# Performance work log

Hardware: AMD Instinct MI355X
Metric: run time of the kernel (lower is better)

Reference implementation:

```python
import jax, jax.numpy as jnp
import numpy as np

H_DIM = 256
N_HEADS = 8
HALF = H_DIM // 2

def _lin(x, W, b):
    # torch nn.Linear: y = x @ W.T + b
    y = x @ W.T
    return y + b if b is not None else y

def setup_inputs() -> dict:
    key = jax.random.key(0)
    ks = jax.random.split(key, 16)
    s = 0.02
    d = {
        'x': jax.random.normal(ks[0], (16, H_DIM, 32, 32), jnp.float32),
        'q1_w': jax.random.normal(ks[1], (HALF, HALF), jnp.float32) * s,
        'q1_b': jnp.zeros((HALF,), jnp.float32),
        'q2_w': jax.random.normal(ks[2], (HALF, HALF), jnp.float32) * s,
        'q2_b': jnp.zeros((HALF,), jnp.float32),
        'k1_w': jax.random.normal(ks[3], (HALF, HALF), jnp.float32) * s,
        'k1_b': jnp.zeros((HALF,), jnp.float32),
        'k2_w': jax.random.normal(ks[4], (HALF, HALF), jnp.float32) * s,
        'k2_b': jnp.zeros((HALF,), jnp.float32),
        'v1_w': jax.random.normal(ks[5], (HALF, HALF), jnp.float32) * s,
        'v1_b': jnp.zeros((HALF,), jnp.float32),
        'v2_w': jax.random.normal(ks[6], (HALF, HALF), jnp.float32) * s,
        'v2_b': jnp.zeros((HALF,), jnp.float32),
        'proj1_w': jax.random.normal(ks[7], (HALF, HALF), jnp.float32) * s,
        'proj1_b': jnp.zeros((HALF,), jnp.float32),
        'proj2_w': jax.random.normal(ks[8], (HALF, HALF), jnp.float32) * s,
        'proj2_b': jnp.zeros((HALF,), jnp.float32),
        'logit_scale': jnp.log(10.0 * jnp.ones((N_HEADS, 1, 1), jnp.float32)),
        'mlp_w1': jax.random.normal(ks[9], (128, 2), jnp.float32) * s,
        'mlp_b1': jnp.zeros((128,), jnp.float32),
        'mlp_w2': jax.random.normal(ks[10], (N_HEADS, 128), jnp.float32) * s,
    }
    return d

def _rel_pos_index(h, w):
    # static (numpy) relative position index, shape [N, N]
    ch, cw = np.meshgrid(np.arange(h), np.arange(w), indexing='ij')
    coords = np.stack([ch.reshape(-1), cw.reshape(-1)])  # [2, N]
    rel = coords[:, :, None] - coords[:, None, :]         # [2, N, N]
    rel = rel.transpose(1, 2, 0)
    rel[:, :, 0] += h - 1
    rel[:, :, 1] += w - 1
    return rel[:, :, 0] * (2 * w - 1) + rel[:, :, 1]

def _forward(x, q1_w, q1_b, q2_w, q2_b, k1_w, k1_b, k2_w, k2_b,
             v1_w, v1_b, v2_w, v2_b, proj1_w, proj1_b, proj2_w, proj2_b,
             logit_scale, mlp_w1, mlp_b1, mlp_w2):
    b, c, h, w = x.shape
    N = h * w
    nh = N_HEADS
    hd = c // nh
    x3 = jnp.transpose(x, (0, 2, 3, 1)).reshape(b, N, c)
    x0, x1 = x3[..., :c // 2], x3[..., c // 2:]

    def qkv(W0, b0, W1, b1):
        t = jnp.concatenate([x0 + _lin(x0, W0, b0), x1 + _lin(x1, W1, b1)], axis=-1)
        return t.reshape(b, N, nh, hd).transpose(0, 2, 1, 3)  # [b, nh, N, hd]

    q = qkv(q1_w, q1_b, q2_w, q2_b)
    k = qkv(k1_w, k1_b, k2_w, k2_b)
    v = qkv(v1_w, v1_b, v2_w, v2_b)

    eps = 1e-12
    qn = q / jnp.maximum(jnp.linalg.norm(q, axis=-1, keepdims=True), eps)
    kn = k / jnp.maximum(jnp.linalg.norm(k, axis=-1, keepdims=True), eps)
    attn = jnp.einsum('bhnd,bhmd->bhnm', qn, kn)  # cosine similarity
    scale = jnp.exp(jnp.minimum(logit_scale, jnp.log(1.0 / 0.01)))  # [nh,1,1]
    attn = attn * scale[None]

    # continuous relative-position bias (CPB) table via small MLP
    rch = jnp.arange(-(h - 1), h, dtype=jnp.float32) / (h - 1 + 1e-8)
    rcw = jnp.arange(-(w - 1), w, dtype=jnp.float32) / (w - 1 + 1e-8)
    gh, gw = jnp.meshgrid(rch, rcw, indexing='ij')
    tab = jnp.stack([gh, gw], axis=-1) * 3.2               # [2h-1, 2w-1, 2]
    tab = jnp.sign(tab) * (1.0 - jnp.exp(-jnp.abs(tab)))
    tab = jax.nn.relu(_lin(tab, mlp_w1, mlp_b1))
    tab = _lin(tab, mlp_w2, None).reshape(-1, nh)          # [(2h-1)(2w-1), nh]

    idx = jnp.asarray(_rel_pos_index(h, w))                # [N, N]
    bias = tab[idx.reshape(-1)].reshape(N, N, nh).transpose(2, 0, 1)
    bias = 16.0 * jax.nn.sigmoid(bias)
    attn = attn + bias[None]

    attn = jax.nn.softmax(attn, axis=-1)
    out = jnp.einsum('bhnm,bhmd->bhnd', attn, v).transpose(0, 2, 1, 3).reshape(b, N, c)
    o0, o1 = out[..., :c // 2], out[..., c // 2:]
    out = jnp.concatenate([_lin(o0, proj1_w, proj1_b), _lin(o1, proj2_w, proj2_b)], axis=-1)
    return out.reshape(b, h, w, c).transpose(0, 3, 1, 2)

def reference(x, q1_w, q1_b, q2_w, q2_b, k1_w, k1_b, k2_w, k2_b,
              v1_w, v1_b, v2_w, v2_b, proj1_w, proj1_b, proj2_w, proj2_b,
              logit_scale, mlp_w1, mlp_b1, mlp_w2):
    return _forward(x, q1_w, q1_b, q2_w, q2_b, k1_w, k1_b, k2_w, k2_b,
                    v1_w, v1_b, v2_w, v2_b, proj1_w, proj1_b, proj2_w, proj2_b,
                    logit_scale, mlp_w1, mlp_b1, mlp_w2)
```

## Files before the change

### kernel.cpp

```cpp
#include <hip/hip_runtime.h>
#include <cmath>


typedef _Float16 half_t;
typedef __attribute__((ext_vector_type(4))) _Float16 half4;
typedef __attribute__((ext_vector_type(8))) _Float16 half8;
typedef __attribute__((ext_vector_type(4))) float float4v;

static __device__ __forceinline__ float4v mfma16(half8 a, half8 b, float4v c) {
  return __builtin_amdgcn_mfma_f32_16x16x32_f16(a, b, c, 0, 0, 0);
}

struct PtrArr8 { const float* p[8]; };

__global__ __launch_bounds__(256) void prep_w(PtrArr8 wsrc, PtrArr8 bsrc,
                                              half_t* __restrict__ wf,
                                              float* __restrict__ bws) {
  int y = blockIdx.y;
  const float* src = nullptr;
  const float* bs = nullptr;
#pragma unroll
  for (int i = 0; i < 8; i++)
    if (i == y) { src = wsrc.p[i]; bs = bsrc.p[i]; }
  int i0 = (blockIdx.x * 256 + threadIdx.x) * 4;
  float4 w = *(const float4*)(src + i0);
  int j = i0 >> 7, k = i0 & 127;
  float id0 = 0.f, id1 = 0.f, id2 = 0.f, id3 = 0.f;
  if (y < 6) {
    if (j == k)     id0 = 1.0f;
    if (j == k + 1) id1 = 1.0f;
    if (j == k + 2) id2 = 1.0f;
    if (j == k + 3) id3 = 1.0f;
  }
  half4 h;
  h[0] = (half_t)(w.x + id0);
  h[1] = (half_t)(w.y + id1);
  h[2] = (half_t)(w.z + id2);
  h[3] = (half_t)(w.w + id3);
  *(half4*)(wf + y * 16384 + i0) = h;
  if (blockIdx.x == 0 && threadIdx.x < 128)
    bws[y * 128 + threadIdx.x] = bs[threadIdx.x];
}

__global__ __launch_bounds__(256) void bias_mlp(const float* __restrict__ w1,
                                                const float* __restrict__ b1,
                                                const float* __restrict__ w2,
                                                float* __restrict__ tabh) {
  __shared__ float sw1[256];
  __shared__ float sb1[128];
  __shared__ float sw2[1024];
  int t = threadIdx.x;
  sw1[t] = w1[t];
  if (t < 128) sb1[t] = b1[t];
  for (int i = t; i < 1024; i += 256) sw2[i] = w2[i];
  __syncthreads();
  int p = blockIdx.x * 256 + t;
  if (p >= 3969) return;
  int ph = p / 63, pw = p % 63;
  float t0 = (float)(ph - 31) * (3.2f / 31.0f);
  float t1 = (float)(pw - 31) * (3.2f / 31.0f);
  t0 = copysignf(1.0f - __expf(-fabsf(t0)), t0);
  t1 = copysignf(1.0f - __expf(-fabsf(t1)), t1);
  float acc[8];
#pragma unroll
  for (int hh = 0; hh < 8; hh++) acc[hh] = 0.0f;
  for (int j = 0; j < 128; j++) {
    float hj = fmaxf(0.0f, t0 * sw1[2 * j] + t1 * sw1[2 * j + 1] + sb1[j]);
#pragma unroll
    for (int hh = 0; hh < 8; hh++) acc[hh] += hj * sw2[hh * 128 + j];
  }
#pragma unroll
  for (int hh = 0; hh < 8; hh++)
    tabh[hh * 3969 + p] = 16.0f / (1.0f + __expf(-acc[hh]));
}

__global__ __launch_bounds__(256) void qkv_mfma(
    const float* __restrict__ x, const half_t* __restrict__ wf,
    const float* __restrict__ lscale, const float* __restrict__ bws,
    half_t* __restrict__ qf, half_t* __restrict__ kf,
    half_t* __restrict__ vf) {
  __shared__ half_t wb[128 * 136];
  __shared__ half_t tbuf[128 * 68];
  int t = threadIdx.x;
  int lane = t & 63, wv = t >> 6, l = lane & 15, quad = lane >> 4;
  int hf = blockIdx.y;
  int m0 = blockIdx.x * 64;
  int b = m0 >> 10, n0 = m0 & 1023;

  half8 afr[4];
  {
    const float* xb = x + (size_t)b * 256 * 1024 + n0 + wv * 16 + l;
#pragma unroll
    for (int ks = 0; ks < 4; ks++) {
      int kbase = hf * 128 + ks * 32 + quad * 8;
      half8 a;
#pragma unroll
      for (int j = 0; j < 8; j++)
        a[j] = (half_t)xb[(size_t)(kbase + j) * 1024];
      afr[ks] = a;
    }
  }

  for (int op = 0; op < 3; op++) {
    int combo = op * 2 + hf;
    __syncthreads();
    {
      const half_t* wg = wf + combo * 16384;
#pragma unroll
      for (int i = 0; i < 8; i++) {
        int flat = (t + 256 * i) * 8;
        int row = flat >> 7, col = flat & 127;
        *(half8*)(wb + row * 136 + col) = *(const half8*)(wg + flat);
      }
    }
    __syncthreads();

    float4v acc[8];
#pragma unroll
    for (int ng = 0; ng < 8; ng++) {
      float4v c = {0.f, 0.f, 0.f, 0.f};
#pragma unroll
      for (int ks = 0; ks < 4; ks++) {
        half8 bfrag =
            *(const half8*)(wb + (ng * 16 + l) * 136 + ks * 32 + quad * 8);
        c = mfma16(afr[ks], bfrag, c);
      }
      acc[ng] = c;
    }
#pragma unroll
    for (int ng = 0; ng < 8; ng++) {
      float bb = bws[combo * 128 + ng * 16 + l];
#pragma unroll
      for (int r2 = 0; r2 < 4; r2++) acc[ng][r2] += bb;
    }
    if (op < 2) {
#pragma unroll
      for (int hg = 0; hg < 4; hg++) {
        float sc = 1.0f;
        if (op == 0)
          sc = __expf(fminf(lscale[hf * 4 + hg], 4.6051702f));
#pragma unroll
        for (int r2 = 0; r2 < 4; r2++) {
          float ss = acc[2 * hg][r2] * acc[2 * hg][r2] +
                     acc[2 * hg + 1][r2] * acc[2 * hg + 1][r2];
          ss += __shfl_xor(ss, 1, 64);
          ss += __shfl_xor(ss, 2, 64);
          ss += __shfl_xor(ss, 4, 64);
          ss += __shfl_xor(ss, 8, 64);
          float rn = sc / fmaxf(sqrtf(ss), 1e-12f);
          acc[2 * hg][r2] *= rn;
          acc[2 * hg + 1][r2] *= rn;
        }
      }
#pragma unroll
      for (int ng = 0; ng < 8; ng++)
#pragma unroll
        for (int r2 = 0; r2 < 4; r2++)
          tbuf[(wv * 16 + quad * 4 + r2) * 132 + ng * 16 + l] =
              (half_t)acc[ng][r2];
      __syncthreads();
      half_t* dst = (op == 0) ? qf : kf;
#pragma unroll
      for (int i = 0; i < 4; i++) {
        int idx = t + 256 * i;
        int row = idx >> 4, colc = (idx & 15) * 8;
        half8 vv = *(const half8*)(tbuf + row * 132 + colc);
        int head = hf * 4 + (colc >> 5), d = colc & 31;
        *(half8*)(dst + (((size_t)b * 8 + head) * 1024 + n0 + row) * 32 + d) =
            vv;
      }
    } else {
#pragma unroll
      for (int ng = 0; ng < 8; ng++) {
        int col = ng * 16 + l;
        half4 hv;
#pragma unroll
        for (int r2 = 0; r2 < 4; r2++) hv[r2] = (half_t)acc[ng][r2];
        *(half4*)(tbuf + col * 68 + wv * 16 + quad * 4) = hv;
      }
      __syncthreads();
#pragma unroll
      for (int i = 0; i < 16; i++) {
        int idx = t + 256 * i;
        int col = idx >> 5, rp = idx & 31;
        unsigned int val = *(const unsigned int*)(tbuf + col * 68 + rp * 2);
        int head = hf * 4 + (col >> 5);
        int d = col & 31;
        *(unsigned int*)((char*)vf +
                         (((((size_t)b * 8 + head) * 32 + d) * 1024) + n0 +
                          rp * 2) * 2) = val;
      }
    }
  }
}

__global__ __launch_bounds__(256) void attn_mfma(
    const half_t* __restrict__ qf, const half_t* __restrict__ kf,
    const half_t* __restrict__ vf, const float* __restrict__ tabh,
    const float* __restrict__ lscale, half_t* __restrict__ ao) {
  __shared__ half_t kb[64 * 40];
  __shared__ half_t vt[32 * 72];
  __shared__ half_t pa[4 * 16 * 72];
  __shared__ float sbias[192];

  int t = threadIdx.x;
  int lane = t & 63, wv = t >> 6, l = lane & 15, quad = lane >> 4;
  int qt = blockIdx.x, h = blockIdx.y, b = blockIdx.z;
  int n0 = qt * 64;
  size_t bh = (size_t)b * 8 + h;
  float scale = __expf(fminf(lscale[h], 4.6051702f));
  float c14 = 14.0f - (scale + 16.0f) * 1.44269504f;

  half8 qfr =
      *(const half8*)(qf + (bh * 1024 + n0 + wv * 16 + l) * 32 + quad * 8);

  int qrow_loc = wv * 16 + l;
  int iwq = qrow_loc & 31;
  int ihl = qrow_loc >> 5;

  float run_l = 0.0f;
  float4v o0 = {0.f, 0.f, 0.f, 0.f}, o1 = {0.f, 0.f, 0.f, 0.f};
  half_t* paw = pa + wv * 16 * 72;

  int key_s = t >> 2, dg_s = t & 3;
  int vd_s = t >> 3, kg_s = t & 7;
  int r3 = (t >= 126) ? 2 : ((t >= 63) ? 1 : 0);
  int pw_s = t - r3 * 63;

  half8 kreg = *(const half8*)(kf + (bh * 1024 + key_s) * 32 + dg_s * 8);
  half8 vreg = *(const half8*)(vf + (bh * 32 + vd_s) * 1024 + kg_s * 8);
  float breg = 0.0f;
  if (t < 189) breg = tabh[h * 3969 + (2 * qt + 30 + r3) * 63 + pw_s];

  for (int kt = 0; kt < 16; kt++) {
    *(half8*)(kb + key_s * 40 + dg_s * 8) = kreg;
    *(half8*)(vt + vd_s * 72 + kg_s * 8) = vreg;
    if (t < 189) sbias[t] = breg;
    __syncthreads();
    if (kt < 15) {
      kreg = *(const half8*)(kf +
                             (bh * 1024 + (kt + 1) * 64 + key_s) * 32 +
                             dg_s * 8);
      vreg = *(const half8*)(vf + (bh * 32 + vd_s) * 1024 + (kt + 1) * 64 +
                             kg_s * 8);
      if (t < 189)
        breg = tabh[h * 3969 + (2 * (qt - kt - 1) + 30 + r3) * 63 + pw_s];
    }

    float4v s[4];
#pragma unroll
    for (int nt = 0; nt < 4; nt++) {
      int base = (ihl - (nt >> 1) + 1) * 63 + iwq + 31 -
                 ((nt & 1) * 16 + 4 * quad);
      float4v c;
      c[0] = sbias[base];
      c[1] = sbias[base - 1];
      c[2] = sbias[base - 2];
      c[3] = sbias[base - 3];
      half8 kfr = *(const half8*)(kb + (nt * 16 + l) * 40 + quad * 8);
      s[nt] = mfma16(kfr, qfr, c);
    }
#pragma unroll
    for (int nt = 0; nt < 4; nt++) {
      half4 ph;
#pragma unroll
      for (int r2 = 0; r2 < 4; r2++) {
        float p = exp2f(fmaf(s[nt][r2], 1.44269504f, c14));
        run_l += p;
        ph[r2] = (half_t)p;
      }
      *(half4*)(paw + l * 72 + nt * 16 + quad * 4) = ph;
    }
#pragma unroll
    for (int ks = 0; ks < 2; ks++) {
      half8 pfr = *(const half8*)(paw + l * 72 + ks * 32 + quad * 8);
      half8 v0f = *(const half8*)(vt + l * 72 + ks * 32 + quad * 8);
      half8 v1f = *(const half8*)(vt + (16 + l) * 72 + ks * 32 + quad * 8);
      o0 = mfma16(pfr, v0f, o0);
      o1 = mfma16(pfr, v1f, o1);
    }
    __syncthreads();
  }

  run_l += __shfl_xor(run_l, 16, 64);
  run_l += __shfl_xor(run_l, 32, 64);
  float rli = 1.0f / run_l;

#pragma unroll
  for (int r2 = 0; r2 < 4; r2++) {
    float linv = __shfl(rli, 20 * quad + r2, 64);
    size_t rowaddr =
        ((size_t)b * 1024 + n0 + wv * 16 + quad * 4 + r2) * 256 + h * 32;
    ao[rowaddr + l] = (half_t)(o0[r2] * linv);
    ao[rowaddr + 16 + l] = (half_t)(o1[r2] * linv);
  }
}

__global__ __launch_bounds__(256) void proj_mfma(
    const half_t* __restrict__ ao, const half_t* __restrict__ wp,
    const float* __restrict__ bws, float* __restrict__ out) {
  __shared__ half_t wb[128 * 136];
  __shared__ float yt[128 * 68];
  int t = threadIdx.x;
  int lane = t & 63, wv = t >> 6, l = lane & 15, quad = lane >> 4;
  int hf = blockIdx.y;
  int m0 = blockIdx.x * 64;
  int b = m0 >> 10, n0 = m0 & 1023;

  {
    const half_t* wg = wp + hf * 16384;
#pragma unroll
    for (int i = 0; i < 8; i++) {
      int flat = (t + 256 * i) * 8;
      int row = flat >> 7, col = flat & 127;
      *(half8*)(wb + row * 136 + col) = *(const half8*)(wg + flat);
    }
  }

  half8 afr[4];
  const half_t* ab =
      ao + ((size_t)m0 + wv * 16 + l) * 256 + hf * 128 + quad * 8;
#pragma unroll
  for (int ks = 0; ks < 4; ks++) afr[ks] = *(const half8*)(ab + ks * 32);
  __syncthreads();

#pragma unroll
  for (int ng = 0; ng < 8; ng++) {
    float4v c = {0.f, 0.f, 0.f, 0.f};
#pragma unroll
    for (int ks = 0; ks < 4; ks++)
      c = mfma16(afr[ks],
                 *(const half8*)(wb + (ng * 16 + l) * 136 + ks * 32 +
                                 quad * 8),
                 c);
    float bb = bws[(6 + hf) * 128 + ng * 16 + l];
#pragma unroll
    for (int r2 = 0; r2 < 4; r2++) c[r2] += bb;
    *(float4v*)(yt + (ng * 16 + l) * 68 + wv * 16 + quad * 4) = c;
  }
  __syncthreads();
#pragma unroll
  for (int i = 0; i < 8; i++) {
    int idx = t + 256 * i;
    int col = idx >> 4, rg = idx & 15;
    float4v vv = *(const float4v*)(yt + col * 68 + rg * 4);
    *(float4v*)(out + ((size_t)b * 256 + hf * 128 + col) * 1024 + n0 +
                rg * 4) = vv;
  }
}

extern "C" void kernel_launch(void* const* d_in, const int* in_sizes, int n_in,
                              void* d_out, int out_size, void* d_ws,
                              size_t ws_size, hipStream_t stream) {
  (void)in_sizes; (void)n_in; (void)out_size; (void)ws_size;
  const float* x = (const float*)d_in[0];

  half_t* ws = (half_t*)d_ws;
  half_t* qfp = ws;
  half_t* kfp = ws + 4194304;
  half_t* vfp = ws + 8388608;
  half_t* aop = ws + 12582912;
  half_t* wfp = ws + 16777216;
  float* tabh = (float*)((char*)d_ws + 33816576);
  float* bws = (float*)((char*)d_ws + 33943584);

  PtrArr8 wsrc, bsrc;
  const int widx[8] = {1, 3, 5, 7, 9, 11, 13, 15};
  for (int i = 0; i < 8; i++) {
    wsrc.p[i] = (const float*)d_in[widx[i]];
    bsrc.p[i] = (const float*)d_in[widx[i] + 1];
  }

  prep_w<<<dim3(16, 8), 256, 0, stream>>>(wsrc, bsrc, wfp, bws);
  bias_mlp<<<16, 256, 0, stream>>>((const float*)d_in[18],
                                   (const float*)d_in[19],
                                   (const float*)d_in[20], tabh);
  qkv_mfma<<<dim3(256, 2), 256, 0, stream>>>(x, wfp, (const float*)d_in[17],
                                             bws, qfp, kfp, vfp);
  attn_mfma<<<dim3(16, 8, 16), 256, 0, stream>>>(
      qfp, kfp, vfp, tabh, (const float*)d_in[17], aop);
  proj_mfma<<<dim3(256, 2), 256, 0, stream>>>(aop, wfp + 6 * 16384, bws,
                                              (float*)d_out);
}
```

Baseline: 193.5 us.

## Restructure attention to 512-query blocks with register K/V and prescaled bias

The attention kernel now launches 512-thread blocks, each covering 512 queries. Every wave holds four 16-row query fragments and reads K/V fragments straight from global memory into registers, so the shared K/V staging and the per-iteration barriers are gone. The relative-position bias slice for the block is loaded once into shared memory. The log2e factor and the max-offset constant are folded into the bias table and into the q scaling upstream, which removes a per-element FMA before exp2. In exchange the grid shrinks to 256 blocks, which risks underfilling the GPU, and K/V global loads are repeated per wave without reuse through LDS.

```diff
diff --git a/kernel.cpp b/kernel.cpp
--- a/kernel.cpp
+++ b/kernel.cpp
@@ -45,7 +45,8 @@
 __global__ __launch_bounds__(256) void bias_mlp(const float* __restrict__ w1,
                                                 const float* __restrict__ b1,
                                                 const float* __restrict__ w2,
-                                                float* __restrict__ tabh) {
+                                                const float* __restrict__ ls,
+                                                float* __restrict__ tabh2) {
   __shared__ float sw1[256];
   __shared__ float sb1[128];
   __shared__ float sw2[1024];
@@ -69,9 +70,14 @@
 #pragma unroll
     for (int hh = 0; hh < 8; hh++) acc[hh] += hj * sw2[hh * 128 + j];
   }
-#pragma unroll
-  for (int hh = 0; hh < 8; hh++)
-    tabh[hh * 3969 + p] = 16.0f / (1.0f + __expf(-acc[hh]));
+  const float L2E = 1.44269504f;
+#pragma unroll
+  for (int hh = 0; hh < 8; hh++) {
+    float scale = __expf(fminf(ls[hh], 4.6051702f));
+    float c14 = 14.0f - (scale + 16.0f) * L2E;
+    float bias = 16.0f / (1.0f + __expf(-acc[hh]));
+    tabh2[hh * 3969 + p] = bias * L2E + c14;
+  }
 }
 
 __global__ __launch_bounds__(256) void qkv_mfma(
@@ -138,7 +144,7 @@
       for (int hg = 0; hg < 4; hg++) {
         float sc = 1.0f;
         if (op == 0)
-          sc = __expf(fminf(lscale[hf * 4 + hg], 4.6051702f));
+          sc = __expf(fminf(lscale[hf * 4 + hg], 4.6051702f)) * 1.44269504f;
 #pragma unroll
         for (int r2 = 0; r2 < 4; r2++) {
           float ss = acc[2 * hg][r2] * acc[2 * hg][r2] +
@@ -194,105 +200,104 @@
   }
 }
 
-__global__ __launch_bounds__(256) void attn_mfma(
+__global__ __launch_bounds__(512) void attn_mfma(
     const half_t* __restrict__ qf, const half_t* __restrict__ kf,
-    const half_t* __restrict__ vf, const float* __restrict__ tabh,
-    const float* __restrict__ lscale, half_t* __restrict__ ao) {
-  __shared__ half_t kb[64 * 40];
-  __shared__ half_t vt[32 * 72];
-  __shared__ half_t pa[4 * 16 * 72];
-  __shared__ float sbias[192];
+    const half_t* __restrict__ vf, const float* __restrict__ tabh2,
+    half_t* __restrict__ ao) {
+  __shared__ float sb2[47 * 63];
+  __shared__ half_t pa[8 * 16 * 80];
 
   int t = threadIdx.x;
   int lane = t & 63, wv = t >> 6, l = lane & 15, quad = lane >> 4;
-  int qt = blockIdx.x, h = blockIdx.y, b = blockIdx.z;
-  int n0 = qt * 64;
+  int qh = blockIdx.x, h = blockIdx.y, b = blockIdx.z;
   size_t bh = (size_t)b * 8 + h;
-  float scale = __expf(fminf(lscale[h], 4.6051702f));
-  float c14 = 14.0f - (scale + 16.0f) * 1.44269504f;
-
-  half8 qfr =
-      *(const half8*)(qf + (bh * 1024 + n0 + wv * 16 + l) * 32 + quad * 8);
-
-  int qrow_loc = wv * 16 + l;
-  int iwq = qrow_loc & 31;
-  int ihl = qrow_loc >> 5;
-
-  float run_l = 0.0f;
-  float4v o0 = {0.f, 0.f, 0.f, 0.f}, o1 = {0.f, 0.f, 0.f, 0.f};
-  half_t* paw = pa + wv * 16 * 72;
-
-  int key_s = t >> 2, dg_s = t & 3;
-  int vd_s = t >> 3, kg_s = t & 7;
-  int r3 = (t >= 126) ? 2 : ((t >= 63) ? 1 : 0);
-  int pw_s = t - r3 * 63;
-
-  half8 kreg = *(const half8*)(kf + (bh * 1024 + key_s) * 32 + dg_s * 8);
-  half8 vreg = *(const half8*)(vf + (bh * 32 + vd_s) * 1024 + kg_s * 8);
-  float breg = 0.0f;
-  if (t < 189) breg = tabh[h * 3969 + (2 * qt + 30 + r3) * 63 + pw_s];
-
+  const half_t* kbase = kf + bh * 1024 * 32;
+  const half_t* vbase = vf + bh * 32 * 1024;
+
+  for (int i = t; i < 2961; i += 512)
+    sb2[i] = tabh2[h * 3969 + qh * 1008 + i];
+
+  int row0 = qh * 512 + wv * 64;
+  half8 qfr[4];
+#pragma unroll
+  for (int s = 0; s < 4; s++)
+    qfr[s] =
+        *(const half8*)(qf + (bh * 1024 + row0 + s * 16 + l) * 32 + quad * 8);
+
+  float4v o0[4], o1[4];
+  float run_l[4];
+#pragma unroll
+  for (int s = 0; s < 4; s++) {
+    o0[s] = (float4v){0.f, 0.f, 0.f, 0.f};
+    o1[s] = (float4v){0.f, 0.f, 0.f, 0.f};
+    run_l[s] = 0.0f;
+  }
+  half_t* paw = pa + wv * 16 * 80;
+  __syncthreads();
+
+#pragma unroll 2
   for (int kt = 0; kt < 16; kt++) {
-    *(half8*)(kb + key_s * 40 + dg_s * 8) = kreg;
-    *(half8*)(vt + vd_s * 72 + kg_s * 8) = vreg;
-    if (t < 189) sbias[t] = breg;
-    __syncthreads();
-    if (kt < 15) {
-      kreg = *(const half8*)(kf +
-                             (bh * 1024 + (kt + 1) * 64 + key_s) * 32 +
-                             dg_s * 8);
-      vreg = *(const half8*)(vf + (bh * 32 + vd_s) * 1024 + (kt + 1) * 64 +
-                             kg_s * 8);
-      if (t < 189)
-        breg = tabh[h * 3969 + (2 * (qt - kt - 1) + 30 + r3) * 63 + pw_s];
-    }
-
-    float4v s[4];
-#pragma unroll
-    for (int nt = 0; nt < 4; nt++) {
-      int base = (ihl - (nt >> 1) + 1) * 63 + iwq + 31 -
-                 ((nt & 1) * 16 + 4 * quad);
-      float4v c;
-      c[0] = sbias[base];
-      c[1] = sbias[base - 1];
-      c[2] = sbias[base - 2];
-      c[3] = sbias[base - 3];
-      half8 kfr = *(const half8*)(kb + (nt * 16 + l) * 40 + quad * 8);
-      s[nt] = mfma16(kfr, qfr, c);
-    }
-#pragma unroll
-    for (int nt = 0; nt < 4; nt++) {
-      half4 ph;
-#pragma unroll
-      for (int r2 = 0; r2 < 4; r2++) {
-        float p = exp2f(fmaf(s[nt][r2], 1.44269504f, c14));
-        run_l += p;
-        ph[r2] = (half_t)p;
-      }
-      *(half4*)(paw + l * 72 + nt * 16 + quad * 4) = ph;
-    }
+    half8 kfr[4], v0fr[2], v1fr[2];
+#pragma unroll
+    for (int nt = 0; nt < 4; nt++)
+      kfr[nt] =
+          *(const half8*)(kbase + (kt * 64 + nt * 16 + l) * 32 + quad * 8);
 #pragma unroll
     for (int ks = 0; ks < 2; ks++) {
-      half8 pfr = *(const half8*)(paw + l * 72 + ks * 32 + quad * 8);
-      half8 v0f = *(const half8*)(vt + l * 72 + ks * 32 + quad * 8);
-      half8 v1f = *(const half8*)(vt + (16 + l) * 72 + ks * 32 + quad * 8);
-      o0 = mfma16(pfr, v0f, o0);
-      o1 = mfma16(pfr, v1f, o1);
-    }
-    __syncthreads();
-  }
-
-  run_l += __shfl_xor(run_l, 16, 64);
-  run_l += __shfl_xor(run_l, 32, 64);
-  float rli = 1.0f / run_l;
-
-#pragma unroll
-  for (int r2 = 0; r2 < 4; r2++) {
-    float linv = __shfl(rli, 20 * quad + r2, 64);
-    size_t rowaddr =
-        ((size_t)b * 1024 + n0 + wv * 16 + quad * 4 + r2) * 256 + h * 32;
-    ao[rowaddr + l] = (half_t)(o0[r2] * linv);
-    ao[rowaddr + 16 + l] = (half_t)(o1[r2] * linv);
+      v0fr[ks] = *(const half8*)(vbase + l * 1024 + kt * 64 + ks * 32 +
+                                 quad * 8);
+      v1fr[ks] = *(const half8*)(vbase + (16 + l) * 1024 + kt * 64 + ks * 32 +
+                                 quad * 8);
+    }
+#pragma unroll
+    for (int s = 0; s < 4; s++) {
+      int ihl = 2 * wv + (s >> 1);
+      float4v sres[4];
+#pragma unroll
+      for (int nt = 0; nt < 4; nt++) {
+        int base = (ihl - 2 * kt - (nt >> 1) + 31) * 63 + (s & 1) * 16 + l +
+                   31 - (nt & 1) * 16 - quad * 4;
+        float4v c;
+        c[0] = sb2[base];
+        c[1] = sb2[base - 1];
+        c[2] = sb2[base - 2];
+        c[3] = sb2[base - 3];
+        sres[nt] = mfma16(kfr[nt], qfr[s], c);
+      }
+#pragma unroll
+      for (int nt = 0; nt < 4; nt++) {
+        half4 ph;
+#pragma unroll
+        for (int r2 = 0; r2 < 4; r2++) {
+          float p = exp2f(sres[nt][r2]);
+          run_l[s] += p;
+          ph[r2] = (half_t)p;
+        }
+        *(half4*)(paw + l * 80 + nt * 16 + quad * 4) = ph;
+      }
+#pragma unroll
+      for (int ks = 0; ks < 2; ks++) {
+        half8 pfr = *(const half8*)(paw + l * 80 + ks * 32 + quad * 8);
+        o0[s] = mfma16(pfr, v0fr[ks], o0[s]);
+        o1[s] = mfma16(pfr, v1fr[ks], o1[s]);
+      }
+    }
+  }
+
+#pragma unroll
+  for (int s = 0; s < 4; s++) {
+    float rl = run_l[s];
+    rl += __shfl_xor(rl, 16, 64);
+    rl += __shfl_xor(rl, 32, 64);
+    float rli = 1.0f / rl;
+#pragma unroll
+    for (int r2 = 0; r2 < 4; r2++) {
+      float linv = __shfl(rli, 20 * quad + r2, 64);
+      size_t rowaddr =
+          ((size_t)b * 1024 + row0 + s * 16 + quad * 4 + r2) * 256 + h * 32;
+      ao[rowaddr + l] = (half_t)(o0[s][r2] * linv);
+      ao[rowaddr + 16 + l] = (half_t)(o1[s][r2] * linv);
+    }
   }
 }
 
@@ -361,7 +366,7 @@
   half_t* vfp = ws + 8388608;
   half_t* aop = ws + 12582912;
   half_t* wfp = ws + 16777216;
-  float* tabh = (float*)((char*)d_ws + 33816576);
+  float* tabh2 = (float*)((char*)d_ws + 33816576);
   float* bws = (float*)((char*)d_ws + 33943584);
 
   PtrArr8 wsrc, bsrc;
@@ -374,11 +379,11 @@
   prep_w<<<dim3(16, 8), 256, 0, stream>>>(wsrc, bsrc, wfp, bws);
   bias_mlp<<<16, 256, 0, stream>>>((const float*)d_in[18],
                                    (const float*)d_in[19],
-                                   (const float*)d_in[20], tabh);
+                                   (const float*)d_in[20],
+                                   (const float*)d_in[17], tabh2);
   qkv_mfma<<<dim3(256, 2), 256, 0, stream>>>(x, wfp, (const float*)d_in[17],
                                              bws, qfp, kfp, vfp);
-  attn_mfma<<<dim3(16, 8, 16), 256, 0, stream>>>(
-      qfp, kfp, vfp, tabh, (const float*)d_in[17], aop);
+  attn_mfma<<<dim3(2, 8, 16), 512, 0, stream>>>(qfp, kfp, vfp, tabh2, aop);
   proj_mfma<<<dim3(256, 2), 256, 0, stream>>>(aop, wfp + 6 * 16384, bws,
                                               (float*)d_out);
 }
```

Measured after the change: 194.7 us. Within noise of the previous version (+0.6%).
